# Optimization experiments

Measured on AMD Instinct MI355X. Metric: run time of the kernel, lower is better.

The kernel has to match this reference:

```python
import jax, jax.numpy as jnp
from jax import lax
import numpy as np

B, L, D_MODEL = 4, 2048, 1024
D_STATE, D_CONV, EXPAND = 16, 4, 2
D_INNER = EXPAND * D_MODEL          # 2048
DT_RANK = D_MODEL // 16             # 64
LN_EPS = 1e-5


def setup_inputs() -> dict:
    key = jax.random.key(0)
    ks = jax.random.split(key, 8)
    s = 0.02
    # S4D-real init for A_log, as in Mamba
    A_init = jnp.tile(jnp.arange(1, D_STATE + 1, dtype=jnp.float32), (D_INNER, 1))
    return {
        "x": jax.random.normal(ks[0], (B, L, D_MODEL), jnp.float32),
        "ln_g": jnp.ones((D_MODEL,), jnp.float32),
        "ln_b": jnp.zeros((D_MODEL,), jnp.float32),
        "W_in": jax.random.normal(ks[1], (D_MODEL, 2 * D_INNER), jnp.float32) * s,
        "conv_w": jax.random.normal(ks[2], (D_INNER, D_CONV), jnp.float32) * s,
        "conv_b": jnp.zeros((D_INNER,), jnp.float32),
        "W_x": jax.random.normal(ks[3], (D_INNER, DT_RANK + 2 * D_STATE), jnp.float32) * s,
        "W_dt": jax.random.normal(ks[4], (DT_RANK, D_INNER), jnp.float32) * s,
        "b_dt": jnp.full((D_INNER,), -4.6, jnp.float32),  # softplus(b_dt) ~ 0.01
        "A_log": jnp.log(A_init),
        "Dskip": jnp.ones((D_INNER,), jnp.float32),
        "W_out": jax.random.normal(ks[5], (D_INNER, D_MODEL), jnp.float32) * s,
    }


def _layer_norm(x, g, b):
    mu = jnp.mean(x, -1, keepdims=True)
    var = jnp.mean((x - mu) ** 2, -1, keepdims=True)
    return (x - mu) * lax.rsqrt(var + LN_EPS) * g + b


def _mamba_block(x, ln_g, ln_b, W_in, conv_w, conv_b, W_x, W_dt, b_dt, A_log, Dskip, W_out):
    b, l, _ = x.shape
    xn = _layer_norm(x, ln_g, ln_b)

    # in_proj -> (u, z), each (B, L, d_inner)
    xz = xn @ W_in
    u, z = jnp.split(xz, 2, axis=-1)

    # causal depthwise conv over L + SiLU
    u_t = u.transpose(0, 2, 1)                      # (B, d_inner, L)
    k = conv_w[:, None, :]                          # (d_inner, 1, d_conv)
    uc = lax.conv_general_dilated(
        u_t, k, (1,), [(D_CONV - 1, 0)],
        dimension_numbers=("NCH", "OIH", "NCH"),
        feature_group_count=D_INNER,
    ) + conv_b[None, :, None]
    uc = jax.nn.silu(uc).transpose(0, 2, 1)         # (B, L, d_inner)

    # input-dependent dt, B, C
    dbc = uc @ W_x                                  # (B, L, dt_rank + 2*d_state)
    dt_r = dbc[..., :DT_RANK]
    Bs = dbc[..., DT_RANK:DT_RANK + D_STATE]        # (B, L, d_state)
    Cs = dbc[..., DT_RANK + D_STATE:]               # (B, L, d_state)
    dt = jax.nn.softplus(dt_r @ W_dt + b_dt)        # (B, L, d_inner)

    A = -jnp.exp(A_log)                             # (d_inner, d_state)

    def step(h, ins):
        dt_t, B_t, C_t, u_t = ins                   # (b,di),(b,ds),(b,ds),(b,di)
        dA = jnp.exp(dt_t[..., None] * A)           # (b, di, ds)
        h = h * dA + (dt_t * u_t)[..., None] * B_t[:, None, :]
        y = jnp.einsum("bds,bs->bd", h, C_t)
        return h, y

    h0 = jnp.zeros((b, D_INNER, D_STATE), x.dtype)
    xs = (dt.transpose(1, 0, 2), Bs.transpose(1, 0, 2),
          Cs.transpose(1, 0, 2), uc.transpose(1, 0, 2))
    _, ys = lax.scan(step, h0, xs)                  # (L, B, d_inner)
    y = ys.transpose(1, 0, 2) + uc * Dskip          # D skip connection
    y = y * jax.nn.silu(z)                          # gate
    return x + y @ W_out                            # residual (dropout=0)


def reference(x, ln_g, ln_b, W_in, conv_w, conv_b, W_x, W_dt, b_dt, A_log, Dskip, W_out):
    return _mamba_block(x, ln_g, ln_b, W_in, conv_w, conv_b, W_x, W_dt, b_dt, A_log, Dskip, W_out)
```

## Files before the change

kernel.cpp:

```cpp
#include <hip/hip_runtime.h>
#include <hip/hip_bf16.h>

#define BB 4
#define LL 2048
#define DM 1024
#define DI 2048
#define DST 16
#define DTR 64
#define ROWS (BB*LL)
#define NC 32
#define CHUNK (LL/NC)

using bf16x8 = __attribute__((ext_vector_type(8))) __bf16;
using f32x4  = __attribute__((ext_vector_type(4))) float;

#define AS1 __attribute__((address_space(1)))
#define AS3 __attribute__((address_space(3)))

__global__ __launch_bounds__(256) void transpose_all_kernel(
        const float* __restrict__ Wi, const float* __restrict__ Wo,
        const float* __restrict__ Wx, const float* __restrict__ Wd,
        __hip_bfloat16* __restrict__ WiT, __hip_bfloat16* __restrict__ WoT,
        __hip_bfloat16* __restrict__ WxT, __hip_bfloat16* __restrict__ WdT) {
    const int t = blockIdx.x;
    const float* src; __hip_bfloat16* dst; int R, C, Cpad, nx, idx;
    if (t < 4096)      { src = Wi; dst = WiT; R = 1024; C = 4096; Cpad = 4096; nx = 128; idx = t; }
    else if (t < 6144) { src = Wo; dst = WoT; R = 2048; C = 1024; Cpad = 1024; nx = 32;  idx = t - 4096; }
    else if (t < 6400) { src = Wx; dst = WxT; R = 2048; C = 96;   Cpad = 128;  nx = 4;   idx = t - 6144; }
    else               { src = Wd; dst = WdT; R = 64;   C = 2048; Cpad = 2048; nx = 64;  idx = t - 6400; }
    __shared__ float tl[32][33];
    const int c0 = (idx % nx) * 32, r0 = (idx / nx) * 32;
    const int tx = threadIdx.x & 31, ty = threadIdx.x >> 5;
    #pragma unroll
    for (int k = 0; k < 4; k++) {
        const int r = r0 + ty + 8 * k, c = c0 + tx;
        tl[ty + 8 * k][tx] = (r < R && c < C) ? src[(size_t)r * C + c] : 0.f;
    }
    __syncthreads();
    #pragma unroll
    for (int k = 0; k < 4; k++) {
        const int c = c0 + ty + 8 * k, r = r0 + tx;
        if (c < Cpad && r < R) dst[(size_t)c * R + r] = __float2bfloat16(tl[tx][ty + 8 * k]);
    }
}

__global__ __launch_bounds__(256) void ln_bf16_kernel(const float* __restrict__ x,
                                                      const float* __restrict__ g,
                                                      const float* __restrict__ bta,
                                                      __hip_bfloat16* __restrict__ xn) {
    const int row = blockIdx.x;
    const int tid = threadIdx.x;
    const float4 v = ((const float4*)(x + (size_t)row * DM))[tid];
    float s  = v.x + v.y + v.z + v.w;
    float sq = v.x*v.x + v.y*v.y + v.z*v.z + v.w*v.w;
    #pragma unroll
    for (int m = 1; m < 64; m <<= 1) {
        s  += __shfl_xor(s, m);
        sq += __shfl_xor(sq, m);
    }
    __shared__ float ss[4], ssq[4];
    const int w = tid >> 6;
    if ((tid & 63) == 0) { ss[w] = s; ssq[w] = sq; }
    __syncthreads();
    s  = ss[0] + ss[1] + ss[2] + ss[3];
    sq = ssq[0] + ssq[1] + ssq[2] + ssq[3];
    const float mu  = s * (1.f / DM);
    const float var = sq * (1.f / DM) - mu * mu;
    const float rs  = rsqrtf(var + 1e-5f);
    const float4 gv = ((const float4*)g)[tid];
    const float4 bv = ((const float4*)bta)[tid];
    __hip_bfloat16* op = xn + (size_t)row * DM + tid * 4;
    op[0] = __float2bfloat16((v.x - mu) * rs * gv.x + bv.x);
    op[1] = __float2bfloat16((v.y - mu) * rs * gv.y + bv.y);
    op[2] = __float2bfloat16((v.z - mu) * rs * gv.z + bv.z);
    op[3] = __float2bfloat16((v.w - mu) * rs * gv.w + bv.w);
}

template<int MODE>
__global__ __launch_bounds__(256) void mfma_gemm(const __hip_bfloat16* __restrict__ A,
                                                 const __hip_bfloat16* __restrict__ Bt,
                                                 float* __restrict__ O,
                                                 __hip_bfloat16* __restrict__ Oz,
                                                 __hip_bfloat16* __restrict__ Ozb,
                                                 const float* __restrict__ Add,
                                                 int Kstride, int klen) {
    __shared__ __hip_bfloat16 As[2 * 128 * 32];
    __shared__ __hip_bfloat16 Bs[2 * 128 * 32];
    const int tid  = threadIdx.x;
    const int lane = tid & 63;
    const int w    = tid >> 6;

    const int nbx = gridDim.x, nby = gridDim.y;
    const int lid = blockIdx.y * nbx + blockIdx.x;
    const int rpx = nby >> 3;
    const int xcd = lid & 7, sl = lid >> 3;
    const int by  = xcd * rpx + (sl % rpx);
    const int bx  = sl / rpx;

    const int row0 = by * 128, col0 = bx * 128;
    const int wr0 = (w >> 1) * 64, wc0 = (w & 1) * 64;

    f32x4 acc[4][4];
    #pragma unroll
    for (int i = 0; i < 4; i++)
        #pragma unroll
        for (int j = 0; j < 4; j++) acc[i][j] = f32x4{0.f, 0.f, 0.f, 0.f};

    const int fm  = lane & 15;
    const int fqi = lane >> 4;
    const int fqX = ((fqi ^ (fm & 3)) << 3);

    const int kbeg = blockIdx.z * klen;
    for (int k0 = kbeg; k0 < kbeg + klen; k0 += 64) {
        #pragma unroll
        for (int j = 0; j < 4; j++) {
            const int c   = w * 256 + j * 64 + lane;
            const int p   = c >> 9;
            const int row = (c >> 2) & 127;
            const int q   = (c & 3) ^ (row & 3);
            const int gk  = k0 + p * 32 + q * 8;
            __builtin_amdgcn_global_load_lds(
                (const AS1 unsigned int*)(A + (size_t)(row0 + row) * Kstride + gk),
                (AS3 unsigned int*)(As + c * 8), 16, 0, 0);
            __builtin_amdgcn_global_load_lds(
                (const AS1 unsigned int*)(Bt + (size_t)(col0 + row) * Kstride + gk),
                (AS3 unsigned int*)(Bs + c * 8), 16, 0, 0);
        }
        __syncthreads();
        #pragma unroll
        for (int half = 0; half < 2; half++) {
            bf16x8 af[4], bfr[4];
            #pragma unroll
            for (int i = 0; i < 4; i++)
                af[i] = *(const bf16x8*)&As[half * 4096 + (wr0 + i * 16 + fm) * 32 + fqX];
            #pragma unroll
            for (int j = 0; j < 4; j++)
                bfr[j] = *(const bf16x8*)&Bs[half * 4096 + (wc0 + j * 16 + fm) * 32 + fqX];
            #pragma unroll
            for (int i = 0; i < 4; i++)
                #pragma unroll
                for (int j = 0; j < 4; j++)
                    acc[i][j] = __builtin_amdgcn_mfma_f32_16x16x32_bf16(af[i], bfr[j], acc[i][j], 0, 0, 0);
        }
        __syncthreads();
    }

    #pragma unroll
    for (int i = 0; i < 4; i++) {
        #pragma unroll
        for (int j = 0; j < 4; j++) {
            #pragma unroll
            for (int r = 0; r < 4; r++) {
                const int row = row0 + wr0 + i * 16 + (lane >> 4) * 4 + r;
                const int col = col0 + wc0 + j * 16 + fm;
                const float v = acc[i][j][r];
                if (MODE == 0) {
                    if (col0 < DI) Oz[(size_t)row * DI + col] = __float2bfloat16(v);
                    else           Ozb[(size_t)row * DI + (col - DI)] = __float2bfloat16(v);
                } else if (MODE == 2) {
                    O[(size_t)row * DM + col] = v + Add[(size_t)row * DM + col];
                } else if (MODE == 3) {
                    const float t  = v + Add[col];
                    const float sp = (t > 20.f) ? t : __logf(1.f + __expf(t));
                    Oz[(size_t)row * DI + col] = __float2bfloat16(sp);
                } else {
                    O[((size_t)blockIdx.z * ROWS + row) * 128 + col] = v;
                }
            }
        }
    }
}

__global__ __launch_bounds__(256) void dbc_reduce_kernel(const float* __restrict__ pbuf,
                                                         float* __restrict__ dbc,
                                                         __hip_bfloat16* __restrict__ dbc64) {
    const size_t gid = (size_t)blockIdx.x * 256 + threadIdx.x;
    const int    col = gid & 127;
    const size_t row = gid >> 7;
    float sum = 0.f;
    #pragma unroll
    for (int sp = 0; sp < 4; sp++)
        sum += pbuf[((size_t)sp * ROWS + row) * 128 + col];
    if (col < DTR)                   dbc64[row * DTR + col] = __float2bfloat16(sum);
    else if (col < DTR + 2 * DST)    dbc[row * 128 + col] = sum;
}

__global__ __launch_bounds__(256) void conv_silu_kernel(const __hip_bfloat16* __restrict__ u,
                                                        const float* __restrict__ cw,
                                                        const float* __restrict__ cb,
                                                        __hip_bfloat16* __restrict__ uc) {
    const int d  = blockIdx.x * 256 + threadIdx.x;
    const int b  = blockIdx.z;
    const int l0 = blockIdx.y * 16;
    const float w0 = cw[d * 4 + 0], w1 = cw[d * 4 + 1];
    const float w2 = cw[d * 4 + 2], w3 = cw[d * 4 + 3];
    const float bias = cb[d];
    const __hip_bfloat16* up = u + (size_t)(b * LL) * DI + d;
    float x0 = (l0 - 3 >= 0) ? __bfloat162float(up[(size_t)(l0 - 3) * DI]) : 0.f;
    float x1 = (l0 - 2 >= 0) ? __bfloat162float(up[(size_t)(l0 - 2) * DI]) : 0.f;
    float x2 = (l0 - 1 >= 0) ? __bfloat162float(up[(size_t)(l0 - 1) * DI]) : 0.f;
    __hip_bfloat16* op = uc + (size_t)(b * LL + l0) * DI + d;
    #pragma unroll
    for (int i = 0; i < 16; i++) {
        const float x3 = __bfloat162float(up[(size_t)(l0 + i) * DI]);
        const float v  = bias + w0 * x0 + w1 * x1 + w2 * x2 + w3 * x3;
        const float sig = __builtin_amdgcn_rcpf(1.f + __expf(-v));
        op[(size_t)i * DI] = __float2bfloat16(v * sig);
        x0 = x1; x1 = x2; x2 = x3;
    }
}

__global__ __launch_bounds__(256) void scan_pass1_kernel(const __hip_bfloat16* __restrict__ dtb,
                                                         const __hip_bfloat16* __restrict__ uc,
                                                         const float* __restrict__ dbc,
                                                         const float* __restrict__ A_log,
                                                         float* __restrict__ hbuf,
                                                         float* __restrict__ Pbuf) {
    __shared__ float Bsh[CHUNK][16];
    const int tid = threadIdx.x;
    const int d   = blockIdx.x * 256 + tid;
    const int c   = blockIdx.y;
    const int b   = blockIdx.z;
    const size_t row0 = (size_t)b * LL + (size_t)c * CHUNK;

    {
        const int r = tid >> 2, j4 = (tid & 3) * 4;
        *(float4*)&Bsh[r][j4] = *(const float4*)(dbc + (row0 + r) * 128 + DTR + j4);
    }
    float a[DST];
    #pragma unroll
    for (int q = 0; q < 4; q++) {
        const float4 t = *(const float4*)(A_log + (size_t)d * DST + q * 4);
        a[q * 4 + 0] = -__expf(t.x); a[q * 4 + 1] = -__expf(t.y);
        a[q * 4 + 2] = -__expf(t.z); a[q * 4 + 3] = -__expf(t.w);
    }
    __syncthreads();

    const __hip_bfloat16* dtp = dtb + row0 * DI + d;
    const __hip_bfloat16* ucp = uc + row0 * DI + d;

    float h[DST];
    #pragma unroll
    for (int s = 0; s < DST; s++) h[s] = 0.f;
    float sdt = 0.f;
    float dtv = __bfloat162float(dtp[0]), ucv = __bfloat162float(ucp[0]);
    for (int l = 0; l < CHUNK; l++) {
        const int ln = (l + 1 < CHUNK) ? (l + 1) : l;
        const float dtn = __bfloat162float(dtp[(size_t)ln * DI]);
        const float ucn = __bfloat162float(ucp[(size_t)ln * DI]);
        const float dtu = dtv * ucv;
        sdt += dtv;
        #pragma unroll
        for (int s = 0; s < DST; s++) {
            const float dA = __expf(dtv * a[s]);
            h[s] = fmaf(h[s], dA, dtu * Bsh[l][s]);
        }
        dtv = dtn; ucv = ucn;
    }
    float* hp = hbuf + (((size_t)b * NC + c) * DI + d) * DST;
    float* pp = Pbuf + (((size_t)b * NC + c) * DI + d) * DST;
    #pragma unroll
    for (int q = 0; q < 4; q++) {
        *(float4*)&hp[q * 4] = float4{h[q*4+0], h[q*4+1], h[q*4+2], h[q*4+3]};
        *(float4*)&pp[q * 4] = float4{__expf(sdt * a[q*4+0]), __expf(sdt * a[q*4+1]),
                                      __expf(sdt * a[q*4+2]), __expf(sdt * a[q*4+3])};
    }
}

__global__ __launch_bounds__(256) void scan_combine_kernel(float* __restrict__ hbuf,
                                                           const float* __restrict__ Pbuf) {
    const size_t gid  = (size_t)blockIdx.x * 256 + threadIdx.x;
    const size_t b    = gid >> 15;
    const size_t d16s = gid & 32767;
    float H = 0.f;
    #pragma unroll
    for (int c = 0; c < NC; c++) {
        const size_t idx = (b * NC + c) * (DI * DST) + d16s;
        const float hc = hbuf[idx];
        const float Pc = Pbuf[idx];
        hbuf[idx] = H;
        H = hc + Pc * H;
    }
}

__global__ __launch_bounds__(256) void scan_pass3_kernel(const __hip_bfloat16* __restrict__ dtb,
                                                         __hip_bfloat16* uc,
                                                         const __hip_bfloat16* __restrict__ z,
                                                         const float* __restrict__ dbc,
                                                         const float* __restrict__ A_log,
                                                         const float* __restrict__ Dskip,
                                                         const float* __restrict__ hbuf) {
    __shared__ float BC[CHUNK][32];
    const int tid = threadIdx.x;
    const int d   = blockIdx.x * 256 + tid;
    const int c   = blockIdx.y;
    const int b   = blockIdx.z;
    const size_t row0 = (size_t)b * LL + (size_t)c * CHUNK;

    #pragma unroll
    for (int i = 0; i < 2; i++) {
        const int idx = i * 256 + tid;
        const int r = idx >> 3, j4 = (idx & 7) * 4;
        *(float4*)&BC[r][j4] = *(const float4*)(dbc + (row0 + r) * 128 + DTR + j4);
    }
    float a[DST];
    #pragma unroll
    for (int q = 0; q < 4; q++) {
        const float4 t = *(const float4*)(A_log + (size_t)d * DST + q * 4);
        a[q * 4 + 0] = -__expf(t.x); a[q * 4 + 1] = -__expf(t.y);
        a[q * 4 + 2] = -__expf(t.z); a[q * 4 + 3] = -__expf(t.w);
    }
    const float dsk = Dskip[d];
    __syncthreads();

    const __hip_bfloat16* dtp = dtb + row0 * DI + d;
    __hip_bfloat16* ucp = uc + row0 * DI + d;
    const __hip_bfloat16* zp = z + row0 * DI + d;

    float h[DST];
    {
        const float* hp = hbuf + (((size_t)b * NC + c) * DI + d) * DST;
        #pragma unroll
        for (int q = 0; q < 4; q++) {
            const float4 t = *(const float4*)&hp[q * 4];
            h[q*4+0] = t.x; h[q*4+1] = t.y; h[q*4+2] = t.z; h[q*4+3] = t.w;
        }
    }
    float dtv = __bfloat162float(dtp[0]);
    float ucv = __bfloat162float(ucp[0]);
    float zv  = __bfloat162float(zp[0]);
    for (int l = 0; l < CHUNK; l++) {
        const int ln = (l + 1 < CHUNK) ? (l + 1) : l;
        const float dtn = __bfloat162float(dtp[(size_t)ln * DI]);
        const float ucn = __bfloat162float(ucp[(size_t)ln * DI]);
        const float zn  = __bfloat162float(zp[(size_t)ln * DI]);
        const float dtu = dtv * ucv;
        float y = 0.f;
        #pragma unroll
        for (int s = 0; s < DST; s++) {
            const float dA = __expf(dtv * a[s]);
            h[s] = fmaf(h[s], dA, dtu * BC[l][s]);
            y = fmaf(h[s], BC[l][16 + s], y);
        }
        const float yt  = fmaf(ucv, dsk, y);
        const float sig = __builtin_amdgcn_rcpf(1.f + __expf(-zv));
        ucp[(size_t)l * DI] = __float2bfloat16(yt * (zv * sig));
        dtv = dtn; ucv = ucn; zv = zn;
    }
}

extern "C" void kernel_launch(void* const* d_in, const int* in_sizes, int n_in,
                              void* d_out, int out_size, void* d_ws, size_t ws_size,
                              hipStream_t stream) {
    const float* x      = (const float*)d_in[0];
    const float* ln_g   = (const float*)d_in[1];
    const float* ln_b   = (const float*)d_in[2];
    const float* W_in   = (const float*)d_in[3];
    const float* conv_w = (const float*)d_in[4];
    const float* conv_b = (const float*)d_in[5];
    const float* W_x    = (const float*)d_in[6];
    const float* W_dt   = (const float*)d_in[7];
    const float* b_dt   = (const float*)d_in[8];
    const float* A_log  = (const float*)d_in[9];
    const float* Dskip  = (const float*)d_in[10];
    const float* W_out  = (const float*)d_in[11];
    float* out = (float*)d_out;

    const size_t MB = 1024ull * 1024ull;
    char* wsb = (char*)d_ws;
    __hip_bfloat16* ub    = (__hip_bfloat16*)(wsb);
    __hip_bfloat16* z     = (__hip_bfloat16*)(wsb + 32 * MB);
    __hip_bfloat16* uc    = (__hip_bfloat16*)(wsb + 64 * MB);
    __hip_bfloat16* xn    = (__hip_bfloat16*)(wsb + 96 * MB);
    __hip_bfloat16* WinT  = (__hip_bfloat16*)(wsb + 112 * MB);
    __hip_bfloat16* WoutT = (__hip_bfloat16*)(wsb + 120 * MB);
    __hip_bfloat16* WxT   = (__hip_bfloat16*)(wsb + 124 * MB);
    float*          dbc   = (float*)(wsb + 125 * MB);
    float*          hbuf  = (float*)(wsb + 129 * MB);
    float*          Pbuf  = (float*)(wsb + 145 * MB);
    __hip_bfloat16* dbc64 = (__hip_bfloat16*)(wsb + 161 * MB);
    __hip_bfloat16* WdtT  = (__hip_bfloat16*)(wsb + 162 * MB);
    float*          pbuf  = (float*)(wsb + 163 * MB);
    __hip_bfloat16* dtb   = ub;

    transpose_all_kernel<<<6528, 256, 0, stream>>>(W_in, W_out, W_x, W_dt,
                                                   WinT, WoutT, WxT, WdtT);
    ln_bf16_kernel<<<ROWS, 256, 0, stream>>>(x, ln_g, ln_b, xn);
    mfma_gemm<0><<<dim3(32, 64), 256, 0, stream>>>(
        xn, WinT, nullptr, ub, z, nullptr, DM, DM);
    conv_silu_kernel<<<dim3(DI / 256, LL / 16, BB), 256, 0, stream>>>(ub, conv_w, conv_b, uc);
    mfma_gemm<4><<<dim3(1, 64, 4), 256, 0, stream>>>(
        uc, WxT, pbuf, nullptr, nullptr, nullptr, DI, DI / 4);
    dbc_reduce_kernel<<<(ROWS * 128) / 256, 256, 0, stream>>>(pbuf, dbc, dbc64);
    mfma_gemm<3><<<dim3(DI / 128, ROWS / 128), 256, 0, stream>>>(
        dbc64, WdtT, nullptr, dtb, nullptr, b_dt, DTR, DTR);
    scan_pass1_kernel<<<dim3(DI / 256, NC, BB), 256, 0, stream>>>(dtb, uc, dbc, A_log, hbuf, Pbuf);
    scan_combine_kernel<<<(BB * DI * DST) / 256, 256, 0, stream>>>(hbuf, Pbuf);
    scan_pass3_kernel<<<dim3(DI / 256, NC, BB), 256, 0, stream>>>(dtb, uc, z, dbc, A_log, Dskip, hbuf);
    mfma_gemm<2><<<dim3(DM / 128, ROWS / 128), 256, 0, stream>>>(
        uc, WoutT, out, nullptr, nullptr, x, DI, DI);
}
```

Baseline: 435.3 us.

## Add 256x256-tile pipelined MFMA GEMM for in_proj with async LDS staging

Adds a new 512-thread GEMM kernel with 256x256 output tiles, double-buffered direct global-to-LDS loads, XOR-swizzled LDS layout, XCD-aware block remapping and phased MFMA/load interleaving with setprio. It is used only for the in_proj GEMM (8192x4096x1024), replacing the 128x128 tile kernel. The intent is to raise data reuse per tile and overlap memory traffic with MFMA work. In exchange it adds many barriers, higher register pressure (a 128-float accumulator per thread) and fewer blocks (512) in flight.

After: 430.8 us. About the same (-1.0%).

```diff
diff --git a/kernel.cpp b/kernel.cpp
--- a/kernel.cpp
+++ b/kernel.cpp
@@ -154,22 +154,171 @@
                 const int row = row0 + wr0 + i * 16 + (lane >> 4) * 4 + r;
                 const int col = col0 + wc0 + j * 16 + fm;
                 const float v = acc[i][j][r];
+                if (MODE == 2) {
+                    O[(size_t)row * DM + col] = v + Add[(size_t)row * DM + col];
+                } else if (MODE == 3) {
+                    const float t  = v + Add[col];
+                    const float sp = (t > 20.f) ? t : __logf(1.f + __expf(t));
+                    Oz[(size_t)row * DI + col] = __float2bfloat16(sp);
+                } else if (MODE == 4) {
+                    O[((size_t)blockIdx.z * ROWS + row) * 128 + col] = v;
+                }
+            }
+        }
+    }
+}
+
+#define STAGE_A(buf, half, kt) do {                                              \
+    _Pragma("unroll")                                                            \
+    for (int j_ = 0; j_ < 2; j_++) {                                             \
+        const int strip_ = w * 2 + j_;                                           \
+        __builtin_amdgcn_global_load_lds(                                        \
+            (const AS1 unsigned int*)(A + (size_t)(row0 + (half)*128 + strip_*8 + srow) * Kstride + ((kt)*64 + schk*8)), \
+            (AS3 unsigned int*)(&As[buf][half][strip_*8][0] + sldo), 16, 0, 0);  \
+    } } while (0)
+
+#define STAGE_B(buf, half, kt) do {                                              \
+    _Pragma("unroll")                                                            \
+    for (int j_ = 0; j_ < 2; j_++) {                                             \
+        const int strip_ = w * 2 + j_;                                           \
+        __builtin_amdgcn_global_load_lds(                                        \
+            (const AS1 unsigned int*)(Bt + (size_t)(col0 + (half)*128 + strip_*8 + srow) * Kstride + ((kt)*64 + schk*8)), \
+            (AS3 unsigned int*)(&Bs[buf][half][strip_*8][0] + sldo), 16, 0, 0);  \
+    } } while (0)
+
+#define LOAD_A(buf, MH) do {                                                     \
+    _Pragma("unroll")                                                            \
+    for (int i_ = 0; i_ < 4; i_++) {                                             \
+        const int r_ = (MH)*64 + i_*16 + fm;                                     \
+        a_[i_][0] = *(const bf16x8*)&As[buf][wm][r_][((fq    ) ^ (fm & 7)) << 3];\
+        a_[i_][1] = *(const bf16x8*)&As[buf][wm][r_][((fq + 4) ^ (fm & 7)) << 3];\
+    } } while (0)
+
+#define LOAD_B(dst, buf, NP) do {                                                \
+    _Pragma("unroll")                                                            \
+    for (int j_ = 0; j_ < 2; j_++) {                                             \
+        const int c_ = (wn & 1)*64 + (NP)*32 + j_*16 + fm;                       \
+        dst[j_][0] = *(const bf16x8*)&Bs[buf][wn >> 1][c_][((fq    ) ^ (fm & 7)) << 3]; \
+        dst[j_][1] = *(const bf16x8*)&Bs[buf][wn >> 1][c_][((fq + 4) ^ (fm & 7)) << 3]; \
+    } } while (0)
+
+#define MFMA_Q(MH, NP, bset) do {                                                \
+    __builtin_amdgcn_s_setprio(1);                                               \
+    _Pragma("unroll")                                                            \
+    for (int i_ = 0; i_ < 4; i_++)                                               \
+        _Pragma("unroll")                                                        \
+        for (int j_ = 0; j_ < 2; j_++) {                                         \
+            acc[(MH)*4+i_][(NP)*2+j_] = __builtin_amdgcn_mfma_f32_16x16x32_bf16( \
+                a_[i_][0], bset[j_][0], acc[(MH)*4+i_][(NP)*2+j_], 0, 0, 0);     \
+            acc[(MH)*4+i_][(NP)*2+j_] = __builtin_amdgcn_mfma_f32_16x16x32_bf16( \
+                a_[i_][1], bset[j_][1], acc[(MH)*4+i_][(NP)*2+j_], 0, 0, 0);     \
+        }                                                                        \
+    __builtin_amdgcn_s_setprio(0);                                               \
+} while (0)
+
+#define PH_SYNC() do {                                                           \
+    __builtin_amdgcn_s_barrier();                                                \
+    asm volatile("s_waitcnt lgkmcnt(0)" ::: "memory");                           \
+} while (0)
+
+template<int MODE>
+__global__ __launch_bounds__(512, 2) void mfma_gemm256(
+        const __hip_bfloat16* __restrict__ A,
+        const __hip_bfloat16* __restrict__ Bt,
+        float* __restrict__ O,
+        __hip_bfloat16* __restrict__ Oz,
+        __hip_bfloat16* __restrict__ Ozb,
+        const float* __restrict__ Add,
+        int Kstride, int K) {
+    __shared__ __hip_bfloat16 As[2][2][128][64];
+    __shared__ __hip_bfloat16 Bs[2][2][128][64];
+    const int tid  = threadIdx.x;
+    const int lane = tid & 63;
+    const int w    = tid >> 6;
+    const int wm   = w >> 2;
+    const int wn   = w & 3;
+    const int fm   = lane & 15;
+    const int fq   = lane >> 4;
+
+    const int nbx = gridDim.x, nby = gridDim.y;
+    const int lid = blockIdx.y * nbx + blockIdx.x;
+    const int rpx = nby >> 3;
+    const int xcd = lid & 7, sl = lid >> 3;
+    const int by  = xcd * rpx + (sl % rpx);
+    const int bx  = sl / rpx;
+    const int row0 = by * 256, col0 = bx * 256;
+
+    const int srow = lane >> 3;
+    const int schk = (lane & 7) ^ srow;
+    const int sldo = lane * 8;
+
+    f32x4 acc[8][4];
+    #pragma unroll
+    for (int i = 0; i < 8; i++)
+        #pragma unroll
+        for (int j = 0; j < 4; j++) acc[i][j] = f32x4{0.f, 0.f, 0.f, 0.f};
+
+    bf16x8 a_[4][2], b0_[2][2], b1_[2][2];
+
+    STAGE_A(0, 0, 0); STAGE_A(0, 1, 0); STAGE_B(0, 0, 0); STAGE_B(0, 1, 0);
+    STAGE_A(1, 0, 1); STAGE_A(1, 1, 1); STAGE_B(1, 0, 1);
+    asm volatile("s_waitcnt vmcnt(6)" ::: "memory");
+    __builtin_amdgcn_s_barrier();
+
+    const int nt = K >> 6;
+    for (int t = 0; t < nt; ++t) {
+        const int buf = t & 1, ob = buf ^ 1;
+        LOAD_A(buf, 0);
+        LOAD_B(b0_, buf, 0);
+        if (t + 1 < nt) STAGE_B(ob, 1, t + 1);
+        PH_SYNC();
+        MFMA_Q(0, 0, b0_);
+        __builtin_amdgcn_s_barrier();
+        LOAD_B(b1_, buf, 1);
+        PH_SYNC();
+        MFMA_Q(0, 1, b1_);
+        __builtin_amdgcn_s_barrier();
+        LOAD_A(buf, 1);
+        if (t + 2 < nt) STAGE_B(buf, 0, t + 2);
+        PH_SYNC();
+        MFMA_Q(1, 1, b1_);
+        __builtin_amdgcn_s_barrier();
+        if (t + 2 < nt) {
+            STAGE_A(buf, 0, t + 2); STAGE_A(buf, 1, t + 2);
+            asm volatile("s_waitcnt vmcnt(6)" ::: "memory");
+        } else {
+            asm volatile("s_waitcnt vmcnt(0)" ::: "memory");
+        }
+        __builtin_amdgcn_s_barrier();
+        MFMA_Q(1, 0, b0_);
+        __builtin_amdgcn_s_barrier();
+    }
+
+    #pragma unroll
+    for (int i = 0; i < 8; i++) {
+        #pragma unroll
+        for (int j = 0; j < 4; j++) {
+            #pragma unroll
+            for (int r = 0; r < 4; r++) {
+                const int row = row0 + wm * 128 + i * 16 + fq * 4 + r;
+                const int col = col0 + wn * 64 + j * 16 + fm;
+                const float v = acc[i][j][r];
                 if (MODE == 0) {
                     if (col0 < DI) Oz[(size_t)row * DI + col] = __float2bfloat16(v);
                     else           Ozb[(size_t)row * DI + (col - DI)] = __float2bfloat16(v);
                 } else if (MODE == 2) {
                     O[(size_t)row * DM + col] = v + Add[(size_t)row * DM + col];
-                } else if (MODE == 3) {
-                    const float t  = v + Add[col];
-                    const float sp = (t > 20.f) ? t : __logf(1.f + __expf(t));
-                    Oz[(size_t)row * DI + col] = __float2bfloat16(sp);
-                } else {
-                    O[((size_t)blockIdx.z * ROWS + row) * 128 + col] = v;
                 }
             }
         }
     }
 }
+#undef STAGE_A
+#undef STAGE_B
+#undef LOAD_A
+#undef LOAD_B
+#undef MFMA_Q
+#undef PH_SYNC
 
 __global__ __launch_bounds__(256) void dbc_reduce_kernel(const float* __restrict__ pbuf,
                                                          float* __restrict__ dbc,
@@ -386,7 +535,7 @@
     transpose_all_kernel<<<6528, 256, 0, stream>>>(W_in, W_out, W_x, W_dt,
                                                    WinT, WoutT, WxT, WdtT);
     ln_bf16_kernel<<<ROWS, 256, 0, stream>>>(x, ln_g, ln_b, xn);
-    mfma_gemm<0><<<dim3(32, 64), 256, 0, stream>>>(
+    mfma_gemm256<0><<<dim3(16, 32), 512, 0, stream>>>(
         xn, WinT, nullptr, ub, z, nullptr, DM, DM);
     conv_silu_kernel<<<dim3(DI / 256, LL / 16, BB), 256, 0, stream>>>(ub, conv_w, conv_b, uc);
     mfma_gemm<4><<<dim3(1, 64, 4), 256, 0, stream>>>(
```
